# Kernel tuning notes

Measured on AMD Instinct MI355X. Metric: run time of the kernel, lower is better.

The kernel has to match this reference:

```python
import jax, jax.numpy as jnp
import numpy as np

B, N, NB, NORB = 8, 128, 32, 128  # batch, particles, single-body basis size, orbitals


def _offdiag_idx(n):
    # [N, N-1] indices of j != i, matching remove_diag with an aux (feature) axis
    return np.stack([np.concatenate([np.arange(i), np.arange(i + 1, n)]) for i in range(n)])


def setup_inputs() -> dict:
    key = jax.random.key(0)
    k1, k2 = jax.random.split(key)
    chi = jax.random.normal(k1, (B, N, NB), dtype=jnp.float32)
    # param('backflow_coeff', normal(stddev=0.01), (Nb*Nb, n_orbitals))
    backflow_coeff = 0.01 * jax.random.normal(k2, (NB * NB, NORB), dtype=jnp.float32)
    return {"chi": chi, "backflow_coeff": backflow_coeff}


def reference(chi, backflow_coeff):
    b, n, nb = chi.shape
    # basis_combine_backflow: chi_munu_ij[b,i,j, k*Nb + l] = chi[b,j,k] * chi[b,i,l]
    # (meshgrid(a=chi_i, b=chi_j) with indexing='xy' -> prod[k,l] = chi_i[l]*chi_j[k], raveled)
    pair = jnp.einsum('bjk,bil->bijkl', chi, chi).reshape(b, n, n, nb * nb)
    # remove_diag(..., has_aux_axis=True): drop j == i along axis 2 -> [B, N, N-1, Nb^2]
    idx = jnp.asarray(_offdiag_idx(n))
    pair = pair[:, jnp.arange(n)[:, None], idx, :]
    # mean over neighbors j != i -> [B, N, Nb^2]
    basis = pair.mean(axis=-2)
    # BF = basis @ backflow_coeff -> [B, N, n_orbitals]
    return basis @ backflow_coeff
```

## Files before the change

### kernel.cpp

```cpp
#include <hip/hip_runtime.h>
#include <hip/hip_bf16.h>

#define B_    8
#define N_    128
#define NB_   32
#define NORB_ 128
#define RPB   4
#define THREADS 1024
#define QG    32

#define P_DW(kl) ((kl) * 4 + ((kl) >> 5) * 4)

__global__ __launch_bounds__(THREADS, 4) void bobf_kernel(
    const float* __restrict__ chi,
    const float* __restrict__ W,
    float* __restrict__ out)
{
    __shared__ float Sp[32][NB_];
    __shared__ float S[NB_];
    __shared__ float x[RPB][NB_];
    __shared__ __align__(16) float p[1024 * 4 + 32 * 4];
    __shared__ float red[QG][RPB][NORB_];

    const int t  = threadIdx.x;
    const int b  = blockIdx.x >> 5;
    const int i0 = (blockIdx.x & 31) * RPB;

    {
        const int k = t & 31;
        const int g = t >> 5;
        const float* base = chi + (b * N_) * NB_ + k;
        float s = 0.f;
        #pragma unroll
        for (int jj = 0; jj < 4; ++jj)
            s += base[(g * 4 + jj) * NB_];
        Sp[g][k] = s;
    }
    if (t < RPB * NB_) {
        const int r = t >> 5, l = t & 31;
        x[r][l] = chi[(b * N_ + i0 + r) * NB_ + l];
    }
    __syncthreads();
    if (t < NB_) {
        float s = 0.f;
        #pragma unroll
        for (int g = 0; g < 32; ++g) s += Sp[g][t];
        S[t] = s;
    }
    __syncthreads();

    {
        const float inv = 1.0f / (float)(N_ - 1);
        const int kl = t;
        const int k = kl >> 5, l = kl & 31;
        float4 v;
        v.x = (S[k] - x[0][k]) * inv * x[0][l];
        v.y = (S[k] - x[1][k]) * inv * x[1][l];
        v.z = (S[k] - x[2][k]) * inv * x[2][l];
        v.w = (S[k] - x[3][k]) * inv * x[3][l];
        *(float4*)&p[P_DW(kl)] = v;
    }
    __syncthreads();

    const int q  = t >> 5;
    const int og = t & 31;
    const float4* p4 = ((const float4*)p) + q * 33;
    const float4* Wf = ((const float4*)(W + (q * 32) * NORB_)) + og;
    float4 a0 = {0,0,0,0}, a1 = {0,0,0,0}, a2 = {0,0,0,0}, a3 = {0,0,0,0};
    #pragma unroll 8
    for (int j = 0; j < 32; ++j) {
        const float4 pv = p4[j];
        const float4 wv = Wf[j * 32];
        a0.x += pv.x * wv.x; a0.y += pv.x * wv.y; a0.z += pv.x * wv.z; a0.w += pv.x * wv.w;
        a1.x += pv.y * wv.x; a1.y += pv.y * wv.y; a1.z += pv.y * wv.z; a1.w += pv.y * wv.w;
        a2.x += pv.z * wv.x; a2.y += pv.z * wv.y; a2.z += pv.z * wv.z; a2.w += pv.z * wv.w;
        a3.x += pv.w * wv.x; a3.y += pv.w * wv.y; a3.z += pv.w * wv.z; a3.w += pv.w * wv.w;
    }
    *(float4*)&red[q][0][og * 4] = a0;
    *(float4*)&red[q][1][og * 4] = a1;
    *(float4*)&red[q][2][og * 4] = a2;
    *(float4*)&red[q][3][og * 4] = a3;
    __syncthreads();

    if (t < RPB * NORB_) {
        const int r = t >> 7, o = t & 127;
        float v = 0.f;
        #pragma unroll
        for (int qq = 0; qq < QG; ++qq) v += red[qq][r][o];
        out[(b * N_ + i0 + r) * NORB_ + o] = v;
    }
}

extern "C" void kernel_launch(void* const* d_in, const int* in_sizes, int n_in,
                              void* d_out, int out_size, void* d_ws, size_t ws_size,
                              hipStream_t stream) {
    const float* chi = (const float*)d_in[0];
    const float* W   = (const float*)d_in[1];
    float* out = (float*)d_out;
    dim3 grid(B_ * (N_ / RPB));
    dim3 block(THREADS);
    hipLaunchKernelGGL(bobf_kernel, grid, block, 0, stream, chi, W, out);
}
```

Before: 11.85 us.

## Retile blocks over rows and output columns, compute pair products in registers

Each block now covers 32 rows and 16 output orbitals instead of 4 rows and all 128 orbitals, with grid still 256 blocks. This cuts per-block W traffic to a column slice and reuses it across more rows. The pair-basis tile is no longer materialised in shared memory; each thread forms y*x products on the fly from a transposed chi tile, which removes one barrier and the large p buffer. The trade-off is a different reduction layout with padded rows and extra multiplies per inner iteration.

```diff
diff --git a/kernel.cpp b/kernel.cpp
--- a/kernel.cpp
+++ b/kernel.cpp
@@ -1,15 +1,14 @@
 #include <hip/hip_runtime.h>
-#include <hip/hip_bf16.h>
 
 #define B_    8
 #define N_    128
 #define NB_   32
 #define NORB_ 128
-#define RPB   4
+#define RPB   32
+#define OPB   16
+#define NQ    32
 #define THREADS 1024
-#define QG    32
-
-#define P_DW(kl) ((kl) * 4 + ((kl) >> 5) * 4)
+#define RPAD  20
 
 __global__ __launch_bounds__(THREADS, 4) void bobf_kernel(
     const float* __restrict__ chi,
@@ -18,13 +17,16 @@
 {
     __shared__ float Sp[32][NB_];
     __shared__ float S[NB_];
-    __shared__ float x[RPB][NB_];
-    __shared__ __align__(16) float p[1024 * 4 + 32 * 4];
-    __shared__ float red[QG][RPB][NORB_];
+    __shared__ __align__(16) float xT[NB_][RPB];
+    __shared__ __align__(16) float red[NQ][RPB][RPAD];
 
-    const int t  = threadIdx.x;
-    const int b  = blockIdx.x >> 5;
-    const int i0 = (blockIdx.x & 31) * RPB;
+    const int t   = threadIdx.x;
+    const int blk = blockIdx.x;
+    const int b    = blk >> 5;
+    const int rowg = (blk >> 3) & 3;
+    const int og   = blk & 7;
+    const int i0   = rowg * RPB;
+    const int o0   = og * OPB;
 
     {
         const int k = t & 31;
@@ -32,13 +34,12 @@
         const float* base = chi + (b * N_) * NB_ + k;
         float s = 0.f;
         #pragma unroll
-        for (int jj = 0; jj < 4; ++jj)
-            s += base[(g * 4 + jj) * NB_];
+        for (int jj = 0; jj < 4; ++jj) s += base[(g * 4 + jj) * NB_];
         Sp[g][k] = s;
     }
-    if (t < RPB * NB_) {
-        const int r = t >> 5, l = t & 31;
-        x[r][l] = chi[(b * N_ + i0 + r) * NB_ + l];
+    {
+        const int l = t >> 5, r = t & 31;
+        xT[l][r] = chi[(b * N_ + i0 + r) * NB_ + l];
     }
     __syncthreads();
     if (t < NB_) {
@@ -49,45 +50,55 @@
     }
     __syncthreads();
 
+    const int q  = t >> 5;
+    const int w_ = t & 31;
+    const int rg = w_ >> 2;
+    const int oq = w_ & 3;
+    const int r0 = rg * 4;
+
+    const float inv = 1.0f / (float)(N_ - 1);
+    float4 yv;
     {
-        const float inv = 1.0f / (float)(N_ - 1);
-        const int kl = t;
-        const int k = kl >> 5, l = kl & 31;
-        float4 v;
-        v.x = (S[k] - x[0][k]) * inv * x[0][l];
-        v.y = (S[k] - x[1][k]) * inv * x[1][l];
-        v.z = (S[k] - x[2][k]) * inv * x[2][l];
-        v.w = (S[k] - x[3][k]) * inv * x[3][l];
-        *(float4*)&p[P_DW(kl)] = v;
+        const float4 xq = *(const float4*)&xT[q][r0];
+        const float Sq = S[q];
+        yv.x = (Sq - xq.x) * inv;
+        yv.y = (Sq - xq.y) * inv;
+        yv.z = (Sq - xq.z) * inv;
+        yv.w = (Sq - xq.w) * inv;
     }
-    __syncthreads();
 
-    const int q  = t >> 5;
-    const int og = t & 31;
-    const float4* p4 = ((const float4*)p) + q * 33;
-    const float4* Wf = ((const float4*)(W + (q * 32) * NORB_)) + og;
+    const float4* Wf = (const float4*)(W + (q * 32) * NORB_ + o0 + oq * 4);
+    const float*  xjp = &xT[0][r0];
+
     float4 a0 = {0,0,0,0}, a1 = {0,0,0,0}, a2 = {0,0,0,0}, a3 = {0,0,0,0};
     #pragma unroll 8
     for (int j = 0; j < 32; ++j) {
-        const float4 pv = p4[j];
-        const float4 wv = Wf[j * 32];
-        a0.x += pv.x * wv.x; a0.y += pv.x * wv.y; a0.z += pv.x * wv.z; a0.w += pv.x * wv.w;
-        a1.x += pv.y * wv.x; a1.y += pv.y * wv.y; a1.z += pv.y * wv.z; a1.w += pv.y * wv.w;
-        a2.x += pv.z * wv.x; a2.y += pv.z * wv.y; a2.z += pv.z * wv.z; a2.w += pv.z * wv.w;
-        a3.x += pv.w * wv.x; a3.y += pv.w * wv.y; a3.z += pv.w * wv.z; a3.w += pv.w * wv.w;
+        const float4 xv = *(const float4*)(xjp + j * RPB);
+        const float4 wv = Wf[j * (NORB_ / 4)];
+        const float p0 = yv.x * xv.x;
+        const float p1 = yv.y * xv.y;
+        const float p2 = yv.z * xv.z;
+        const float p3 = yv.w * xv.w;
+        a0.x += p0 * wv.x; a0.y += p0 * wv.y; a0.z += p0 * wv.z; a0.w += p0 * wv.w;
+        a1.x += p1 * wv.x; a1.y += p1 * wv.y; a1.z += p1 * wv.z; a1.w += p1 * wv.w;
+        a2.x += p2 * wv.x; a2.y += p2 * wv.y; a2.z += p2 * wv.z; a2.w += p2 * wv.w;
+        a3.x += p3 * wv.x; a3.y += p3 * wv.y; a3.z += p3 * wv.z; a3.w += p3 * wv.w;
     }
-    *(float4*)&red[q][0][og * 4] = a0;
-    *(float4*)&red[q][1][og * 4] = a1;
-    *(float4*)&red[q][2][og * 4] = a2;
-    *(float4*)&red[q][3][og * 4] = a3;
+
+    {
+        float* rq = &red[q][0][0] + oq * 4;
+        *(float4*)&rq[(r0 + 0) * RPAD] = a0;
+        *(float4*)&rq[(r0 + 1) * RPAD] = a1;
+        *(float4*)&rq[(r0 + 2) * RPAD] = a2;
+        *(float4*)&rq[(r0 + 3) * RPAD] = a3;
+    }
     __syncthreads();
-
-    if (t < RPB * NORB_) {
-        const int r = t >> 7, o = t & 127;
+    if (t < RPB * OPB) {
+        const int r = t >> 4, o = t & 15;
         float v = 0.f;
         #pragma unroll
-        for (int qq = 0; qq < QG; ++qq) v += red[qq][r][o];
-        out[(b * N_ + i0 + r) * NORB_ + o] = v;
+        for (int qq = 0; qq < NQ; ++qq) v += red[qq][r][o];
+        out[(b * N_ + i0 + r) * NORB_ + o0 + o] = v;
     }
 }
 
@@ -97,7 +108,7 @@
     const float* chi = (const float*)d_in[0];
     const float* W   = (const float*)d_in[1];
     float* out = (float*)d_out;
-    dim3 grid(B_ * (N_ / RPB));
+    dim3 grid(256);
     dim3 block(THREADS);
     hipLaunchKernelGGL(bobf_kernel, grid, block, 0, stream, chi, W, out);
 }
```

Result: no change. 11.93 us (+0.7%).
